# Optimization experiments

Measured on AMD Instinct MI355X. Metric: run time of the kernel, lower is better.

The kernel has to match this reference:

```python
import jax, jax.numpy as jnp
import numpy as np

# Per-channel class frequencies from the original module (23 AU channels)
_W = np.array([0.0012597430655963838, 0.0004919313290455535, 0.0021106513104319356,
               0.0007678117365508301, 0.004719881670572202, 0.000372272357115554,
               0.029090425620315438, 0.010056339432617042, 0.0034817436971298467,
               0.0003057951504877765, 0.003995280118329428, 8.808229878180519e-05,
               0.012070598793438699, 0.016788818533845208, 0.0017832510677901316,
               0.0008758371973209686, 0.0005933090691529143, 0.0031992155689617922,
               0.003212511010287348, 0.0016685778863572154, 0.0009356666832859684,
               0.0010985358395240233, 0.00103372056306194], dtype=np.float32)
_WEIGHT_0 = 1.0 / (_W + 1.0)        # used when target == 0
_WEIGHT_1 = 1.0 - _WEIGHT_0          # used when target == 1

B, C = 1000000, 23

def setup_inputs() -> dict:
    key = jax.random.key(0)
    k1, k2 = jax.random.split(key)
    # probabilities strictly inside (0,1) so log terms stay finite
    x = jax.random.uniform(k1, (B, C), dtype=jnp.float32) * 0.98 + 0.01
    labels = jax.random.randint(k2, (B, C), 0, 2, dtype=jnp.int32)
    return {"x": x, "labels": labels}

def reference(x, labels):
    # target = (labels > 0).float(); the eq(999) mask in the original is computed but unused
    target = (labels > 0).astype(x.dtype)
    w0 = jnp.asarray(_WEIGHT_0, dtype=x.dtype)  # [C]
    w1 = jnp.asarray(_WEIGHT_1, dtype=x.dtype)  # [C]
    # per-element weight: 1/weight_0[ch] if target==0 else 1/weight_1[ch]
    w = jnp.where(target == 0, 1.0 / w0, 1.0 / w1)  # [B, C] via broadcast
    bce = -(target * jnp.log(x) + (1.0 - target) * jnp.log(1.0 - x))
    loss = jnp.sum(w * bce)
    n, c = x.shape
    return loss / (n * c)
```

## Files before the change

### kernel.cpp

```cpp
#include <hip/hip_runtime.h>

#define NCH 23
#define U 4
#define TILE_V4 (64 * U)

constexpr float c_W[NCH] = {
    0.0012597430655963838f, 0.0004919313290455535f, 0.0021106513104319356f,
    0.0007678117365508301f, 0.004719881670572202f,  0.000372272357115554f,
    0.029090425620315438f,  0.010056339432617042f,  0.0034817436971298467f,
    0.0003057951504877765f, 0.003995280118329428f,  8.808229878180519e-05f,
    0.012070598793438699f,  0.016788818533845208f,  0.0017832510677901316f,
    0.0008758371973209686f, 0.0005933090691529143f, 0.0031992155689617922f,
    0.003212511010287348f,  0.0016685778863572154f, 0.0009356666832859684f,
    0.0010985358395240233f, 0.00103372056306194f
};
constexpr float NEG_LN2 = -0.69314718055994530942f;

struct Tabs { float w[2 * NCH]; };
constexpr Tabs make_tabs() {
    Tabs t{};
    for (int c = 0; c < NCH; ++c) {
        float w0 = 1.0f / (c_W[c] + 1.0f);
        float w1 = 1.0f - w0;
        t.w[c]       = (1.0f / w0) * NEG_LN2;
        t.w[NCH + c] = (1.0f / w1) * NEG_LN2;
    }
    return t;
}
__constant__ Tabs d_tabs = make_tabs();

__device__ __forceinline__ unsigned wrap23(unsigned c) {
    return c >= NCH ? c - NCH : c;
}

__device__ __forceinline__ void elem(float xx, int lab, unsigned c,
                                     const float* s_wt, float& acc) {
    bool t  = lab > 0;
    float v = t ? xx : 1.0f - xx;
    float w = s_wt[c + (t ? NCH : 0u)];
    acc = __builtin_fmaf(w, __log2f(v), acc);
}

__global__ __launch_bounds__(256) void bce_reduce_kernel(
        const float4* __restrict__ x4, const int4* __restrict__ l4,
        double* __restrict__ partial, unsigned n4 ) {
    __shared__ float s_wt[2 * NCH];
    if (threadIdx.x < 2 * NCH) s_wt[threadIdx.x] = d_tabs.w[threadIdx.x];
    __syncthreads();

    const unsigned gtid     = blockIdx.x * blockDim.x + threadIdx.x;
    const unsigned nthreads = gridDim.x * blockDim.x;
    const unsigned lane     = threadIdx.x & 63u;
    const unsigned wid      = gtid >> 6;
    const unsigned nwaves   = nthreads >> 6;
    const unsigned ntiles   = n4 / TILE_V4;

    float acc = 0.0f;

    for (unsigned T = wid; T < ntiles; T += nwaves) {
        const unsigned base = T * TILE_V4;
        float4 xv[U];
        int4   lv[U];
        #pragma unroll
        for (int j = 0; j < U; ++j) xv[j] = x4[base + 64u * j + lane];
        #pragma unroll
        for (int j = 0; j < U; ++j) lv[j] = l4[base + 64u * j + lane];

        const unsigned cb = (12u * T + 4u * lane) % NCH;
        #pragma unroll
        for (int j = 0; j < U; ++j) {
            unsigned c = wrap23(cb + (3u * j) % NCH);
            elem(xv[j].x, lv[j].x, c, s_wt, acc); c = wrap23(c + 1);
            elem(xv[j].y, lv[j].y, c, s_wt, acc); c = wrap23(c + 1);
            elem(xv[j].z, lv[j].z, c, s_wt, acc); c = wrap23(c + 1);
            elem(xv[j].w, lv[j].w, c, s_wt, acc);
        }
    }

    for (unsigned v = ntiles * TILE_V4 + gtid; v < n4; v += nthreads) {
        float4 xv = x4[v];
        int4   lv = l4[v];
        unsigned c = (4u * v) % NCH;
        elem(xv.x, lv.x, c, s_wt, acc); c = wrap23(c + 1);
        elem(xv.y, lv.y, c, s_wt, acc); c = wrap23(c + 1);
        elem(xv.z, lv.z, c, s_wt, acc); c = wrap23(c + 1);
        elem(xv.w, lv.w, c, s_wt, acc);
    }

    #pragma unroll
    for (int off = 32; off > 0; off >>= 1) acc += __shfl_down(acc, off, 64);
    __shared__ float s_part[4];
    const int wave = threadIdx.x >> 6;
    if ((threadIdx.x & 63) == 0) s_part[wave] = acc;
    __syncthreads();
    if (threadIdx.x == 0) {
        float s = s_part[0] + s_part[1] + s_part[2] + s_part[3];
        atomicAdd(partial, (double)s);
    }
}

__global__ void bce_finalize_kernel(const double* __restrict__ partial,
                                    float* __restrict__ out, unsigned n) {
    out[0] = (float)(partial[0] / (double)n);
}

extern "C" void kernel_launch(void* const* d_in, const int* in_sizes, int n_in,
                              void* d_out, int out_size, void* d_ws, size_t ws_size,
                              hipStream_t stream) {
    const float* x      = (const float*)d_in[0];
    const int*   labels = (const int*)d_in[1];
    float*       out    = (float*)d_out;
    double*      acc    = (double*)d_ws;
    unsigned n  = (unsigned)in_sizes[0];
    unsigned n4 = n >> 2;

    hipMemsetAsync(acc, 0, sizeof(double), stream);

    const int block = 256;
    const int grid  = 1024;
    bce_reduce_kernel<<<grid, block, 0, stream>>>(
        (const float4*)x, (const int4*)labels, acc, n4);
    bce_finalize_kernel<<<1, 1, 0, stream>>>(acc, out, n);
}
```

Measured before the change: 197.9 us.

## Double-buffer tile loads in grid-stride loop and retune tile and grid size

Prefetches the next tile into a second register buffer while the current tile is being consumed, so global loads overlap the log and FMA work. It halves the per-tile unroll to 2, adds a launch-bounds occupancy hint of 8 blocks, and doubles the grid to 2048 blocks to put more waves in flight for hiding memory latency. The channel-offset arithmetic is updated to match the new tile size. The two buffers raise register pressure, and a larger grid means more atomic adds at the end.

```diff
diff --git a/kernel.cpp b/kernel.cpp
--- a/kernel.cpp
+++ b/kernel.cpp
@@ -1,7 +1,7 @@
 #include <hip/hip_runtime.h>
 
 #define NCH 23
-#define U 4
+#define U 2
 #define TILE_V4 (64 * U)
 
 constexpr float c_W[NCH] = {
@@ -41,7 +41,33 @@
     acc = __builtin_fmaf(w, __log2f(v), acc);
 }
 
-__global__ __launch_bounds__(256) void bce_reduce_kernel(
+struct Buf { float4 xv[U]; int4 lv[U]; };
+
+__device__ __forceinline__ void load_tile(const float4* __restrict__ x4,
+                                          const int4* __restrict__ l4,
+                                          unsigned T, unsigned lane, Buf& b) {
+    const unsigned base = T * TILE_V4 + lane;
+    #pragma unroll
+    for (int j = 0; j < U; ++j) b.xv[j] = x4[base + 64u * j];
+    #pragma unroll
+    for (int j = 0; j < U; ++j) b.lv[j] = l4[base + 64u * j];
+}
+
+__device__ __forceinline__ void consume_tile(const Buf& b, unsigned T,
+                                             unsigned lane, const float* s_wt,
+                                             float& acc) {
+    const unsigned cb = (6u * T + 4u * lane) % NCH;
+    #pragma unroll
+    for (int j = 0; j < U; ++j) {
+        unsigned c = wrap23(cb + 3u * j);
+        elem(b.xv[j].x, b.lv[j].x, c, s_wt, acc); c = wrap23(c + 1);
+        elem(b.xv[j].y, b.lv[j].y, c, s_wt, acc); c = wrap23(c + 1);
+        elem(b.xv[j].z, b.lv[j].z, c, s_wt, acc); c = wrap23(c + 1);
+        elem(b.xv[j].w, b.lv[j].w, c, s_wt, acc);
+    }
+}
+
+__global__ __launch_bounds__(256, 8) void bce_reduce_kernel(
         const float4* __restrict__ x4, const int4* __restrict__ l4,
         double* __restrict__ partial, unsigned n4 ) {
     __shared__ float s_wt[2 * NCH];
@@ -57,23 +83,21 @@
 
     float acc = 0.0f;
 
-    for (unsigned T = wid; T < ntiles; T += nwaves) {
-        const unsigned base = T * TILE_V4;
-        float4 xv[U];
-        int4   lv[U];
-        #pragma unroll
-        for (int j = 0; j < U; ++j) xv[j] = x4[base + 64u * j + lane];
-        #pragma unroll
-        for (int j = 0; j < U; ++j) lv[j] = l4[base + 64u * j + lane];
-
-        const unsigned cb = (12u * T + 4u * lane) % NCH;
-        #pragma unroll
-        for (int j = 0; j < U; ++j) {
-            unsigned c = wrap23(cb + (3u * j) % NCH);
-            elem(xv[j].x, lv[j].x, c, s_wt, acc); c = wrap23(c + 1);
-            elem(xv[j].y, lv[j].y, c, s_wt, acc); c = wrap23(c + 1);
-            elem(xv[j].z, lv[j].z, c, s_wt, acc); c = wrap23(c + 1);
-            elem(xv[j].w, lv[j].w, c, s_wt, acc);
+    Buf b0, b1;
+    unsigned T = wid;
+    if (T < ntiles) {
+        load_tile(x4, l4, T, lane, b0);
+        while (true) {
+            unsigned Tn = T + nwaves;
+            if (Tn >= ntiles) { consume_tile(b0, T, lane, s_wt, acc); break; }
+            load_tile(x4, l4, Tn, lane, b1);
+            consume_tile(b0, T, lane, s_wt, acc);
+            T = Tn;
+            Tn = T + nwaves;
+            if (Tn >= ntiles) { consume_tile(b1, T, lane, s_wt, acc); break; }
+            load_tile(x4, l4, Tn, lane, b0);
+            consume_tile(b1, T, lane, s_wt, acc);
+            T = Tn;
         }
     }
 
@@ -117,7 +141,7 @@
     hipMemsetAsync(acc, 0, sizeof(double), stream);
 
     const int block = 256;
-    const int grid  = 1024;
+    const int grid  = 2048;
     bce_reduce_kernel<<<grid, block, 0, stream>>>(
         (const float4*)x, (const int4*)labels, acc, n4);
     bce_finalize_kernel<<<1, 1, 0, stream>>>(acc, out, n);
```

Measured after the change: 197.2 us. No clear change (-0.4%).
